# Kernel tuning notes

Measured on AMD Instinct MI355X. Metric: run time of the kernel, lower is better.

Reference implementation:

```python
import jax, jax.numpy as jnp
import numpy as np

NUM_LAYERS = 3


def setup_inputs() -> dict:
    key = jax.random.key(0)
    k1, k2, k3 = jax.random.split(key, 3)
    N, D, E = 100000, 64, 1250000
    emb = jax.random.normal(k1, (N, D), dtype=jnp.float32)
    edge_attr = jax.random.uniform(k2, (E,), dtype=jnp.float32)
    edge_index = jax.random.randint(k3, (2, E), 0, N, dtype=jnp.int64)
    return {"emb": emb, "edge_attr": edge_attr, "edge_index": edge_index}


def reference(emb, edge_attr, edge_index):
    # LightGCN.get_embedding with uniform alpha = 1/(num_layers+1)
    N = emb.shape[0]
    src, dst = edge_index[0], edge_index[1]
    # gcn_norm (add_self_loops=False): symmetric normalization of edge weights
    deg = jax.ops.segment_sum(edge_attr, dst, num_segments=N)  # [N]
    dinv = jnp.where(deg > 0, jax.lax.rsqrt(deg), 0.0)
    w = dinv[src] * edge_attr * dinv[dst]  # [E]
    alpha = jnp.float32(1.0 / (NUM_LAYERS + 1))
    x = emb
    out = x * alpha
    for _ in range(NUM_LAYERS):
        # gather source embeddings, scale by normalized weight, scatter-add to dst
        msgs = x[src] * w[:, None]  # [E, D]
        x = jax.ops.segment_sum(msgs, dst, num_segments=N)  # [N, D]
        out = out + x * alpha
    return out
```

## Files before the change

kernel.cpp:

```cpp
#include <hip/hip_runtime.h>
#include <hip/hip_fp16.h>


#define G 256
#define SH 6
#define BNODES 64
#define WINV (1.0f / 32767.0f)

__global__ void __launch_bounds__(256) k_bhist(const int* __restrict__ ei,
                                               int* __restrict__ bcnt, int NB, int E) {
    extern __shared__ unsigned int hist[];
    int g = blockIdx.x, t = threadIdx.x;
    for (int b = t; b < NB; b += 256) hist[b] = 0;
    __syncthreads();
    int chunk = (E + G - 1) / G;
    int lo = g * chunk;
    int hi = min(lo + chunk, E);
    for (int i = lo + t; i < hi; i += 256) {
        int d = ei[E + i];
        atomicAdd(&hist[d >> SH], 1u);
    }
    __syncthreads();
    for (int b = t; b < NB; b += 256) bcnt[b * G + g] = (int)hist[b];
}

__global__ void __launch_bounds__(512) k_scan_local(const int* __restrict__ in,
                                                    int* __restrict__ outExcl,
                                                    int* __restrict__ sums, int n) {
    __shared__ int s[512];
    int t = threadIdx.x;
    int i = blockIdx.x * 512 + t;
    int v = (i < n) ? in[i] : 0;
    s[t] = v;
    __syncthreads();
    for (int off = 1; off < 512; off <<= 1) {
        int x = (t >= off) ? s[t - off] : 0;
        __syncthreads();
        s[t] += x;
        __syncthreads();
    }
    if (i < n) outExcl[i] = s[t] - v;
    if (t == 511) sums[blockIdx.x] = s[511];
}

__global__ void __launch_bounds__(1024) k_scan_partials1024(int* __restrict__ p, int n) {
    __shared__ int s[1024];
    int t = threadIdx.x;
    int v = (t < n) ? p[t] : 0;
    s[t] = v;
    __syncthreads();
    for (int off = 1; off < 1024; off <<= 1) {
        int x = (t >= off) ? s[t - off] : 0;
        __syncthreads();
        s[t] += x;
        __syncthreads();
    }
    if (t < n) p[t] = s[t] - v;
}


__global__ void __launch_bounds__(256) k_bscatter(const int* __restrict__ ei,
                                                  const float* __restrict__ ea,
                                                  const int* __restrict__ sc0,
                                                  const int* __restrict__ sums,
                                                  int2* __restrict__ ebuf, int NB, int E) {
    extern __shared__ unsigned int cur[];
    int g = blockIdx.x, t = threadIdx.x;
    for (int b = t; b < NB; b += 256) {
        int f = b * G + g;
        cur[b] = (unsigned)(sc0[f] + sums[f >> 9]);
    }
    __syncthreads();
    int chunk = (E + G - 1) / G;
    int lo = g * chunk;
    int hi = min(lo + chunk, E);
    for (int i = lo + t; i < hi; i += 256) {
        int srcv = ei[i];
        int d = ei[E + i];
        float w = ea[i];
        unsigned pos = atomicAdd(&cur[d >> SH], 1u);
        int2 m;
        m.x = srcv | ((d & (BNODES - 1)) << 25);
        m.y = __float_as_int(w);
        ebuf[pos] = m;
    }
}

__global__ void __launch_bounds__(256) k_bfinal(const int2* __restrict__ ebuf,
                                                const int* __restrict__ sc0,
                                                const int* __restrict__ sums,
                                                unsigned int* __restrict__ meta,
                                                int* __restrict__ row_start,
                                                float* __restrict__ dinv,
                                                int NB, int N, int E) {
    __shared__ unsigned int hcnt[BNODES];
    __shared__ float hsum[BNODES];
    __shared__ unsigned int hoff[BNODES];
    __shared__ unsigned int cur[BNODES];
    int b = blockIdx.x, t = threadIdx.x;
    if (t < BNODES) {
        hcnt[t] = 0;
        hsum[t] = 0.0f;
    }
    __syncthreads();
    int f0 = b * G;
    int e0 = sc0[f0] + sums[f0 >> 9];
    int e1 = (b + 1 < NB) ? (sc0[f0 + G] + sums[(f0 + G) >> 9]) : E;
    for (int i = e0 + t; i < e1; i += 256) {
        int2 m = ebuf[i];
        int dl = (m.x >> 25) & (BNODES - 1);
        atomicAdd(&hcnt[dl], 1u);
        atomicAdd(&hsum[dl], __int_as_float(m.y));
    }
    __syncthreads();
    if (t == 0) {
        unsigned r = 0;
        for (int k = 0; k < BNODES; ++k) {
            hoff[k] = r;
            r += hcnt[k];
        }
    }
    __syncthreads();
    if (t < BNODES) {
        cur[t] = hoff[t];
        int node = (b << SH) + t;
        if (node < N) {
            row_start[node] = e0 + (int)hoff[t];
            float s = hsum[t];
            dinv[node] = (s > 0.0f) ? rsqrtf(s) : 0.0f;
        }
    }
    if (b == 0 && t == 0) row_start[N] = E;
    __syncthreads();
    for (int i = e0 + t; i < e1; i += 256) {
        int2 m = ebuf[i];
        int dl = (m.x >> 25) & (BNODES - 1);
        unsigned p = atomicAdd(&cur[dl], 1u);
        float w = __int_as_float(m.y);
        unsigned q = (unsigned)__float2int_rn(w * 32767.0f);
        q = min(q, 32767u);
        meta[e0 + (int)p] = (unsigned)(m.x & ((1 << 17) - 1)) | (q << 17);
    }
}

__global__ void k_z0(const float2* __restrict__ emb2, const float* __restrict__ dinv,
                     __half2* __restrict__ z, int n2) {
    int i = blockIdx.x * blockDim.x + threadIdx.x;
    if (i < n2) {
        float s = dinv[i >> 5];
        float2 v = emb2[i];
        z[i] = __floats2half2_rn(v.x * s, v.y * s);
    }
}

union F2H {
    float2 f;
    __half2 h[2];
};

template <int MODE>
__global__ void __launch_bounds__(256) k_prop(const float2* __restrict__ zin,
                                              const unsigned int* __restrict__ meta,
                                              const int* __restrict__ row_start,
                                              const float* __restrict__ dinv,
                                              float2* __restrict__ zout,
                                              const float4* __restrict__ emb,
                                              const float2* __restrict__ z1,
                                              const float2* __restrict__ z2,
                                              float4* __restrict__ out, int N) {
    int g = (blockIdx.x * 256 + threadIdx.x) >> 4;
    if (g >= N) return;
    int l = threadIdx.x & 15;
    int b = row_start[g];
    int e = row_start[g + 1];

    float4 acc = make_float4(0.f, 0.f, 0.f, 0.f);
    int i = b;
    for (; i + 8 <= e; i += 8) {
        unsigned mm[8];
        F2H uu[8];
        #pragma unroll
        for (int k = 0; k < 8; ++k) mm[k] = meta[i + k];
        #pragma unroll
        for (int k = 0; k < 8; ++k) uu[k].f = zin[(size_t)(mm[k] & 0x1FFFFu) * 16 + l];
        #pragma unroll
        for (int k = 0; k < 8; ++k) {
            float w = (float)(mm[k] >> 17) * WINV;
            float2 a = __half22float2(uu[k].h[0]), bb = __half22float2(uu[k].h[1]);
            acc.x = fmaf(a.x, w, acc.x);
            acc.y = fmaf(a.y, w, acc.y);
            acc.z = fmaf(bb.x, w, acc.z);
            acc.w = fmaf(bb.y, w, acc.w);
        }
    }
    for (; i + 4 <= e; i += 4) {
        unsigned mm[4];
        F2H uu[4];
        #pragma unroll
        for (int k = 0; k < 4; ++k) mm[k] = meta[i + k];
        #pragma unroll
        for (int k = 0; k < 4; ++k) uu[k].f = zin[(size_t)(mm[k] & 0x1FFFFu) * 16 + l];
        #pragma unroll
        for (int k = 0; k < 4; ++k) {
            float w = (float)(mm[k] >> 17) * WINV;
            float2 a = __half22float2(uu[k].h[0]), bb = __half22float2(uu[k].h[1]);
            acc.x = fmaf(a.x, w, acc.x);
            acc.y = fmaf(a.y, w, acc.y);
            acc.z = fmaf(bb.x, w, acc.z);
            acc.w = fmaf(bb.y, w, acc.w);
        }
    }
    for (; i < e; ++i) {
        unsigned m = meta[i];
        F2H u;
        u.f = zin[(size_t)(m & 0x1FFFFu) * 16 + l];
        float w = (float)(m >> 17) * WINV;
        float2 a = __half22float2(u.h[0]), bb = __half22float2(u.h[1]);
        acc.x = fmaf(a.x, w, acc.x);
        acc.y = fmaf(a.y, w, acc.y);
        acc.z = fmaf(bb.x, w, acc.z);
        acc.w = fmaf(bb.y, w, acc.w);
    }

    float sd = dinv[g];
    int o = g * 16 + l;
    if (MODE == 0) {
        float s2 = sd * sd;
        F2H u;
        u.h[0] = __floats2half2_rn(s2 * acc.x, s2 * acc.y);
        u.h[1] = __floats2half2_rn(s2 * acc.z, s2 * acc.w);
        zout[o] = u.f;
    } else {
        float rd = (sd > 0.0f) ? (1.0f / sd) : 0.0f;
        F2H u1, u2;
        u1.f = z1[o];
        u2.f = z2[o];
        float2 a1 = __half22float2(u1.h[0]), b1 = __half22float2(u1.h[1]);
        float2 a2 = __half22float2(u2.h[0]), b2 = __half22float2(u2.h[1]);
        float4 ev = emb[o];
        float4 r;
        r.x = 0.25f * (ev.x + rd * (a1.x + a2.x) + sd * acc.x);
        r.y = 0.25f * (ev.y + rd * (a1.y + a2.y) + sd * acc.y);
        r.z = 0.25f * (ev.z + rd * (b1.x + b2.x) + sd * acc.z);
        r.w = 0.25f * (ev.w + rd * (b1.y + b2.y) + sd * acc.w);
        out[o] = r;
    }
}

static inline size_t align_up(size_t x, size_t a) { return (x + a - 1) & ~(a - 1); }

extern "C" void kernel_launch(void* const* d_in, const int* in_sizes, int n_in,
                              void* d_out, int out_size, void* d_ws, size_t ws_size,
                              hipStream_t stream) {
    const float* emb = (const float*)d_in[0];
    const float* ea  = (const float*)d_in[1];
    const int*   ei  = (const int*)d_in[2];
    float* out = (float*)d_out;

    const int D = 64;
    const int N = in_sizes[0] / D;
    const int E = in_sizes[1];

    const int NB = (N + BNODES - 1) / BNODES;
    const int NS = NB * G;
    const int nchunk = (NS + 511) / 512;

    char* ws = (char*)d_ws;
    size_t off = 0;
    int* bcnt = (int*)(ws + off);           off = align_up(off + (size_t)NS * 4, 256);
    int* sc0 = (int*)(ws + off);            off = align_up(off + (size_t)NS * 4, 256);
    int* sums = (int*)(ws + off);           off = align_up(off + 1024 * 4, 256);
    int* row_start = (int*)(ws + off);      off = align_up(off + (size_t)(N + 1) * 4, 256);
    float* dinv = (float*)(ws + off);       off = align_up(off + (size_t)N * 4, 256);
    int2* ebuf = (int2*)(ws + off);         off = align_up(off + (size_t)E * 8, 256);
    unsigned int* meta = (unsigned int*)(ws + off); off = align_up(off + (size_t)E * 4, 256);
    __half2* z0 = (__half2*)(ws + off);     off = align_up(off + (size_t)N * D * 2, 256);
    __half2* z1 = (__half2*)(ws + off);     off = align_up(off + (size_t)N * D * 2, 256);
    __half2* z2 = (__half2*)(ws + off);     off = align_up(off + (size_t)N * D * 2, 256);
    (void)ws_size;

    k_bhist<<<G, 256, NB * 4, stream>>>(ei, bcnt, NB, E);
    k_scan_local<<<nchunk, 512, 0, stream>>>(bcnt, sc0, sums, NS);
    k_scan_partials1024<<<1, 1024, 0, stream>>>(sums, nchunk);
    k_bscatter<<<G, 256, NB * 4, stream>>>(ei, ea, sc0, sums, ebuf, NB, E);
    k_bfinal<<<NB, 256, 0, stream>>>(ebuf, sc0, sums, meta, row_start, dinv, NB, N, E);

    k_z0<<<(N * 32 + 255) / 256, 256, 0, stream>>>((const float2*)emb, dinv, z0, N * 32);

    int lb = (N * 16 + 255) / 256;
    k_prop<0><<<lb, 256, 0, stream>>>((const float2*)z0, meta, row_start, dinv,
                                      (float2*)z1, nullptr, nullptr, nullptr, nullptr, N);
    k_prop<0><<<lb, 256, 0, stream>>>((const float2*)z1, meta, row_start, dinv,
                                      (float2*)z2, nullptr, nullptr, nullptr, nullptr, N);
    k_prop<1><<<lb, 256, 0, stream>>>((const float2*)z2, meta, row_start, dinv,
                                      nullptr, (const float4*)emb, (const float2*)z1,
                                      (const float2*)z2, (float4*)out, N);
}
```

Before: 148.8 us.

## Restructure bucket scan into column prefix plus tiny scan, fuse z0 into bfinal

Transposes the bucket histogram to a group-major layout, then computes per-bucket column prefixes in a thread-per-bucket kernel and scans the bucket totals in one small block. This replaces the two-level global scan over NB*G entries. The z0 scaling kernel is folded into k_bfinal, which now writes dinv-scaled half embeddings for its 64 nodes, saving one launch and a dinv reload. The final output store is made nontemporal. The serial 256-step loop per thread in k_colprefix and the single-block tiled scan add latency in exchange.

```diff
diff --git a/kernel.cpp b/kernel.cpp
--- a/kernel.cpp
+++ b/kernel.cpp
@@ -6,6 +6,8 @@
 #define SH 6
 #define BNODES 64
 #define WINV (1.0f / 32767.0f)
+
+typedef float f4_native __attribute__((ext_vector_type(4)));
 
 __global__ void __launch_bounds__(256) k_bhist(const int* __restrict__ ei,
                                                int* __restrict__ bcnt, int NB, int E) {
@@ -21,55 +23,61 @@
         atomicAdd(&hist[d >> SH], 1u);
     }
     __syncthreads();
-    for (int b = t; b < NB; b += 256) bcnt[b * G + g] = (int)hist[b];
-}
-
-__global__ void __launch_bounds__(512) k_scan_local(const int* __restrict__ in,
-                                                    int* __restrict__ outExcl,
-                                                    int* __restrict__ sums, int n) {
-    __shared__ int s[512];
+    for (int b = t; b < NB; b += 256) bcnt[(size_t)g * NB + b] = (int)hist[b];
+}
+
+__global__ void k_colprefix(const int* __restrict__ bcnt, int* __restrict__ sc0,
+                            int* __restrict__ btot, int NB) {
+    int b = blockIdx.x * blockDim.x + threadIdx.x;
+    if (b >= NB) return;
+    int run = 0;
+    #pragma unroll 8
+    for (int g = 0; g < G; ++g) {
+        int v = bcnt[(size_t)g * NB + b];
+        sc0[(size_t)g * NB + b] = run;
+        run += v;
+    }
+    btot[b] = run;
+}
+
+__global__ void __launch_bounds__(256) k_btot_scan(const int* __restrict__ btot,
+                                                   int* __restrict__ bbase, int NB) {
+    __shared__ int s[256];
+    __shared__ int carry;
     int t = threadIdx.x;
-    int i = blockIdx.x * 512 + t;
-    int v = (i < n) ? in[i] : 0;
-    s[t] = v;
-    __syncthreads();
-    for (int off = 1; off < 512; off <<= 1) {
-        int x = (t >= off) ? s[t - off] : 0;
+    if (t == 0) carry = 0;
+    __syncthreads();
+    int ntile = (NB + 255) / 256;
+    for (int tile = 0; tile < ntile; ++tile) {
+        int i = tile * 256 + t;
+        int v = (i < NB) ? btot[i] : 0;
+        s[t] = v;
         __syncthreads();
-        s[t] += x;
+        for (int off = 1; off < 256; off <<= 1) {
+            int x = (t >= off) ? s[t - off] : 0;
+            __syncthreads();
+            s[t] += x;
+            __syncthreads();
+        }
+        int incl = s[t];
+        int c = carry;
+        if (i < NB) bbase[i] = c + incl - v;
         __syncthreads();
-    }
-    if (i < n) outExcl[i] = s[t] - v;
-    if (t == 511) sums[blockIdx.x] = s[511];
-}
-
-__global__ void __launch_bounds__(1024) k_scan_partials1024(int* __restrict__ p, int n) {
-    __shared__ int s[1024];
-    int t = threadIdx.x;
-    int v = (t < n) ? p[t] : 0;
-    s[t] = v;
-    __syncthreads();
-    for (int off = 1; off < 1024; off <<= 1) {
-        int x = (t >= off) ? s[t - off] : 0;
+        if (t == 255) carry = c + incl;
         __syncthreads();
-        s[t] += x;
-        __syncthreads();
-    }
-    if (t < n) p[t] = s[t] - v;
-}
-
+    }
+    if (t == 0) bbase[NB] = carry;
+}
 
 __global__ void __launch_bounds__(256) k_bscatter(const int* __restrict__ ei,
                                                   const float* __restrict__ ea,
                                                   const int* __restrict__ sc0,
-                                                  const int* __restrict__ sums,
+                                                  const int* __restrict__ bbase,
                                                   int2* __restrict__ ebuf, int NB, int E) {
     extern __shared__ unsigned int cur[];
     int g = blockIdx.x, t = threadIdx.x;
-    for (int b = t; b < NB; b += 256) {
-        int f = b * G + g;
-        cur[b] = (unsigned)(sc0[f] + sums[f >> 9]);
-    }
+    for (int b = t; b < NB; b += 256)
+        cur[b] = (unsigned)(bbase[b] + sc0[(size_t)g * NB + b]);
     __syncthreads();
     int chunk = (E + G - 1) / G;
     int lo = g * chunk;
@@ -87,25 +95,26 @@
 }
 
 __global__ void __launch_bounds__(256) k_bfinal(const int2* __restrict__ ebuf,
-                                                const int* __restrict__ sc0,
-                                                const int* __restrict__ sums,
+                                                const int* __restrict__ bbase,
+                                                const float2* __restrict__ emb2,
                                                 unsigned int* __restrict__ meta,
                                                 int* __restrict__ row_start,
                                                 float* __restrict__ dinv,
+                                                __half2* __restrict__ z0,
                                                 int NB, int N, int E) {
     __shared__ unsigned int hcnt[BNODES];
     __shared__ float hsum[BNODES];
     __shared__ unsigned int hoff[BNODES];
     __shared__ unsigned int cur[BNODES];
+    __shared__ float sdv[BNODES];
     int b = blockIdx.x, t = threadIdx.x;
     if (t < BNODES) {
         hcnt[t] = 0;
         hsum[t] = 0.0f;
     }
     __syncthreads();
-    int f0 = b * G;
-    int e0 = sc0[f0] + sums[f0 >> 9];
-    int e1 = (b + 1 < NB) ? (sc0[f0 + G] + sums[(f0 + G) >> 9]) : E;
+    int e0 = bbase[b];
+    int e1 = bbase[b + 1];
     for (int i = e0 + t; i < e1; i += 256) {
         int2 m = ebuf[i];
         int dl = (m.x >> 25) & (BNODES - 1);
@@ -123,11 +132,13 @@
     __syncthreads();
     if (t < BNODES) {
         cur[t] = hoff[t];
+        float s = hsum[t];
+        float dv = (s > 0.0f) ? rsqrtf(s) : 0.0f;
+        sdv[t] = dv;
         int node = (b << SH) + t;
         if (node < N) {
             row_start[node] = e0 + (int)hoff[t];
-            float s = hsum[t];
-            dinv[node] = (s > 0.0f) ? rsqrtf(s) : 0.0f;
+            dinv[node] = dv;
         }
     }
     if (b == 0 && t == 0) row_start[N] = E;
@@ -141,15 +152,15 @@
         q = min(q, 32767u);
         meta[e0 + (int)p] = (unsigned)(m.x & ((1 << 17) - 1)) | (q << 17);
     }
-}
-
-__global__ void k_z0(const float2* __restrict__ emb2, const float* __restrict__ dinv,
-                     __half2* __restrict__ z, int n2) {
-    int i = blockIdx.x * blockDim.x + threadIdx.x;
-    if (i < n2) {
-        float s = dinv[i >> 5];
-        float2 v = emb2[i];
-        z[i] = __floats2half2_rn(v.x * s, v.y * s);
+    int base = b << SH;
+    for (int idx = t; idx < BNODES * 32; idx += 256) {
+        int node = idx >> 5;
+        int gnode = base + node;
+        if (gnode < N) {
+            float s = sdv[node];
+            float2 v = emb2[(size_t)gnode * 32 + (idx & 31)];
+            z0[(size_t)gnode * 32 + (idx & 31)] = __floats2half2_rn(v.x * s, v.y * s);
+        }
     }
 }
 
@@ -238,12 +249,12 @@
         float2 a1 = __half22float2(u1.h[0]), b1 = __half22float2(u1.h[1]);
         float2 a2 = __half22float2(u2.h[0]), b2 = __half22float2(u2.h[1]);
         float4 ev = emb[o];
-        float4 r;
+        f4_native r;
         r.x = 0.25f * (ev.x + rd * (a1.x + a2.x) + sd * acc.x);
         r.y = 0.25f * (ev.y + rd * (a1.y + a2.y) + sd * acc.y);
         r.z = 0.25f * (ev.z + rd * (b1.x + b2.x) + sd * acc.z);
         r.w = 0.25f * (ev.w + rd * (b1.y + b2.y) + sd * acc.w);
-        out[o] = r;
+        __builtin_nontemporal_store(r, reinterpret_cast<f4_native*>(&out[o]));
     }
 }
 
@@ -263,13 +274,13 @@
 
     const int NB = (N + BNODES - 1) / BNODES;
     const int NS = NB * G;
-    const int nchunk = (NS + 511) / 512;
 
     char* ws = (char*)d_ws;
     size_t off = 0;
     int* bcnt = (int*)(ws + off);           off = align_up(off + (size_t)NS * 4, 256);
     int* sc0 = (int*)(ws + off);            off = align_up(off + (size_t)NS * 4, 256);
-    int* sums = (int*)(ws + off);           off = align_up(off + 1024 * 4, 256);
+    int* btot = (int*)(ws + off);           off = align_up(off + (size_t)NB * 4, 256);
+    int* bbase = (int*)(ws + off);          off = align_up(off + (size_t)(NB + 1) * 4, 256);
     int* row_start = (int*)(ws + off);      off = align_up(off + (size_t)(N + 1) * 4, 256);
     float* dinv = (float*)(ws + off);       off = align_up(off + (size_t)N * 4, 256);
     int2* ebuf = (int2*)(ws + off);         off = align_up(off + (size_t)E * 8, 256);
@@ -280,12 +291,11 @@
     (void)ws_size;
 
     k_bhist<<<G, 256, NB * 4, stream>>>(ei, bcnt, NB, E);
-    k_scan_local<<<nchunk, 512, 0, stream>>>(bcnt, sc0, sums, NS);
-    k_scan_partials1024<<<1, 1024, 0, stream>>>(sums, nchunk);
-    k_bscatter<<<G, 256, NB * 4, stream>>>(ei, ea, sc0, sums, ebuf, NB, E);
-    k_bfinal<<<NB, 256, 0, stream>>>(ebuf, sc0, sums, meta, row_start, dinv, NB, N, E);
-
-    k_z0<<<(N * 32 + 255) / 256, 256, 0, stream>>>((const float2*)emb, dinv, z0, N * 32);
+    k_colprefix<<<(NB + 255) / 256, 256, 0, stream>>>(bcnt, sc0, btot, NB);
+    k_btot_scan<<<1, 256, 0, stream>>>(btot, bbase, NB);
+    k_bscatter<<<G, 256, NB * 4, stream>>>(ei, ea, sc0, bbase, ebuf, NB, E);
+    k_bfinal<<<NB, 256, 0, stream>>>(ebuf, bbase, (const float2*)emb, meta, row_start,
+                                     dinv, z0, NB, N, E);
 
     int lb = (N * 16 + 255) / 256;
     k_prop<0><<<lb, 256, 0, stream>>>((const float2*)z0, meta, row_start, dinv,
```

Result: slower. 155.1 us (+4.2%).
